# Kernel optimization log

Measured on AMD Instinct MI355X. Metric: run time of the kernel, lower is better.

Reference implementation:

```python
import jax, jax.numpy as jnp
import numpy as np

B, S, H, NH, NE = 4, 1024, 256, 4, 4
D = H // NH  # head_unit = 64
EPS = 1e-8


def layernorm(x, g, b):
    m = jnp.mean(x, axis=-1, keepdims=True)
    v = jnp.mean((x - m) ** 2, axis=-1, keepdims=True)
    return (x - m) / jnp.sqrt(v + EPS) * g + b


def setup_inputs() -> dict:
    key = jax.random.key(0)
    ks = jax.random.split(key, 18)
    sc = 0.05
    return {
        "x": jax.random.normal(ks[0], (B, S, H), jnp.float32),
        # MoEMultiHead params
        "hl_w": jax.random.normal(ks[1], (NH, D, H), jnp.float32) * sc,   # head_layer weights (out,in)
        "hl_b": jax.random.normal(ks[2], (NH, D), jnp.float32) * sc,
        "wq": jax.random.normal(ks[3], (NH, NE, D, D), jnp.float32) * sc,  # w_q[i*NH+j] -> wq[i,j]
        "wk": jax.random.normal(ks[4], (NH, D, D), jnp.float32) * sc,
        "wv": jax.random.normal(ks[5], (NH, D, D), jnp.float32) * sc,
        "gate_w": jax.random.normal(ks[6], (NH, NE, NE * D), jnp.float32) * sc,
        "gate_b": jax.random.normal(ks[7], (NH, NE), jnp.float32) * sc,
        "ln_g": jnp.ones((D,), jnp.float32),
        "ln_b": jnp.zeros((D,), jnp.float32),
        # FFN params (built inside forward in torch; materialized here)
        "fc1_w": jax.random.normal(ks[8], (D, D), jnp.float32) * sc,
        "fc1_b": jax.random.normal(ks[9], (D,), jnp.float32) * sc,
        "fc2_w": jax.random.normal(ks[10], (D, D), jnp.float32) * sc,
        "fc2_b": jax.random.normal(ks[11], (D,), jnp.float32) * sc,
        "fnorm_g": jnp.ones((D,), jnp.float32),
        "fnorm_b": jnp.zeros((D,), jnp.float32),
        "fgate_w": jax.random.normal(ks[12], (NH, H), jnp.float32) * sc,
    }


def reference(x, hl_w, hl_b, wq, wk, wv, gate_w, gate_b, ln_g, ln_b,
              fc1_w, fc1_b, fc2_w, fc2_b, fnorm_g, fnorm_b, fgate_w):
    b, s, h = x.shape
    nh, d, _ = wk.shape
    ne = wq.shape[1]
    # per-head projection of full hidden -> head_unit  (B, NH, S, D)
    sx = jnp.einsum('bsh,ndh->bnsd', x, hl_w) + hl_b[None, :, None, :]
    pad = sx == 0  # padding mask, same for all experts
    # per-(head, expert) q; per-head k, v
    q = jnp.einsum('bnsd,neod->bneso', sx, wq)       # (B,NH,NE,S,D)
    k = jnp.einsum('bnsd,nod->bnso', sx, wk)         # (B,NH,S,D)
    v = jnp.einsum('bnsd,nod->bnso', sx, wv)
    causal = jnp.where(jnp.tril(jnp.ones((s, s), bool)), 0.0, -jnp.inf).astype(x.dtype)
    # NOTE: original MULTIPLIES by sqrt(head_unit) (bug-faithful)
    scores = jnp.einsum('bnesd,bntd->bnest', q, k) * (d ** 0.5) + causal
    att = jax.nn.softmax(scores, axis=-1)
    qkv = jnp.einsum('bnest,bntd->bnesd', att, v)
    qkv = jnp.where(pad[:, :, None], 0.0, qkv)
    # concat experts along feature dim: (B,NH,S,NE*D)
    out = jnp.transpose(qkv, (0, 1, 3, 2, 4)).reshape(b, nh, s, ne * d)
    gs = jax.nn.softmax(jnp.einsum('bnsf,nef->bnse', out, gate_w) + gate_b[None, :, None, :], axis=-1)
    mixed = jnp.einsum('bnsed,bnse->bnsd', out.reshape(b, nh, s, ne, d), gs)
    # bug-faithful residual: split_x[i] indexes the BATCH dim with head index i
    resid = sx[jnp.arange(nh), jnp.arange(nh)]  # (NH, S, D), broadcast over batch
    hn = layernorm(mixed + resid, ln_g, ln_b)   # (B,NH,S,D); dropout inactive (p=0)
    f_n = jnp.transpose(hn, (0, 2, 1, 3)).reshape(b, s, h)
    # ---- FFN (fresh module in torch; deterministic params here) ----
    fx = f_n.reshape(b, s, nh, d)  # torch.split along feature dim
    pm = fx == 0
    hx = jnp.where(pm, 0.0, fx @ fc1_w.T + fc1_b)
    hx = jax.nn.relu(hx)
    hx = jnp.where(pm, 0.0, hx @ fc2_w.T + fc2_b)
    hx = layernorm(hx + fx, fnorm_g, fnorm_b)
    fout = hx.reshape(b, s, h)
    fg = jax.nn.softmax(fout @ fgate_w.T, axis=-1)  # (B,S,NH)
    return (fout.reshape(b, s, nh, d) * fg[..., None]).reshape(b, s, h)
```

## Files before the change

### kernel.cpp

```cpp
#include <hip/hip_runtime.h>
#include <math.h>

typedef unsigned short u16;
typedef __attribute__((ext_vector_type(8))) unsigned short us8;
typedef __attribute__((ext_vector_type(4))) unsigned short us4;
typedef __attribute__((ext_vector_type(8))) short bf16x8;
typedef __attribute__((ext_vector_type(4))) float f32x4;

constexpr int B_ = 4, S_ = 1024, H_ = 256, NH_ = 4, NE_ = 4, D_ = 64;
constexpr float EPS_ = 1e-8f;

__device__ __forceinline__ u16 f2bf(float f){
  unsigned u = __float_as_uint(f);
  unsigned rnd = 0x7fffu + ((u>>16)&1u);
  return (u16)((u + rnd)>>16);
}
__device__ __forceinline__ float bf2f(u16 u){ return __uint_as_float(((unsigned)u)<<16); }
__device__ __forceinline__ us4 pack4(float4 a){
  us4 r; r[0]=f2bf(a.x); r[1]=f2bf(a.y); r[2]=f2bf(a.z); r[3]=f2bf(a.w);
  return r;
}
#define MFMA16(a,b,c) __builtin_amdgcn_mfma_f32_16x16x32_bf16((bf16x8)(a),(bf16x8)(b),(c),0,0,0)

__global__ __launch_bounds__(256) void k_sx(const float* __restrict__ x, const float* __restrict__ hlw,
                                            const float* __restrict__ hlb,
                                            float* __restrict__ sx, u16* __restrict__ sxb){
  int mt = blockIdx.x >> 3, nt = blockIdx.x & 7;
  int tid = threadIdx.x, w = tid>>6, l = tid&63, lr = l>>4, lc = l&15;
  __shared__ u16 Xs[64*64];
  __shared__ u16 Ws[32*64];
  const int swl = (lc&7)<<3;
  f32x4 acc[2] = {{0,0,0,0},{0,0,0,0}};
  for(int ks=0; ks<4; ++ks){
    __syncthreads();
    #pragma unroll
    for(int it=0; it<4; ++it){
      int g = tid + it*256; int row = g>>4, c4 = (g&15)*4;
      float4 a = *(const float4*)(x + ((size_t)(mt*64+row))*H_ + ks*64 + c4);
      *(us4*)&Xs[row*64 + (c4 ^ ((row&7)<<3))] = pack4(a);
    }
    #pragma unroll
    for(int it=0; it<2; ++it){
      int g = tid + it*256; int row = g>>4, c4 = (g&15)*4;
      float4 a = *(const float4*)(hlw + ((size_t)(nt*32+row))*H_ + ks*64 + c4);
      *(us4*)&Ws[row*64 + (c4 ^ ((row&7)<<3))] = pack4(a);
    }
    __syncthreads();
    bf16x8 a0 = *(const bf16x8*)&Xs[(w*16+lc)*64 + ((lr*8   ) ^ swl)];
    bf16x8 a1 = *(const bf16x8*)&Xs[(w*16+lc)*64 + ((lr*8+32) ^ swl)];
    #pragma unroll
    for(int j=0;j<2;j++){
      const u16* wr = &Ws[(j*16+lc)*64];
      bf16x8 b0 = *(const bf16x8*)(wr + ((lr*8   ) ^ swl));
      bf16x8 b1 = *(const bf16x8*)(wr + ((lr*8+32) ^ swl));
      acc[j] = MFMA16(a0,b0,acc[j]);
      acc[j] = MFMA16(a1,b1,acc[j]);
    }
  }
  #pragma unroll
  for(int j=0;j<2;j++){
    int col = nt*32 + j*16 + lc;
    int n = col>>6, d = col&63;
    float bias = hlb[col];
    #pragma unroll
    for(int r=0;r<4;r++){
      int m = mt*64 + w*16 + lr*4 + r;
      int b = m>>10, s = m&1023;
      float v = acc[j][r] + bias;
      size_t idx = ((size_t)(b*NH_+n)*S_+s)*D_ + d;
      sx[idx] = v; sxb[idx] = f2bf(v);
    }
  }
}

__global__ __launch_bounds__(256) void k_qkv(const u16* __restrict__ sxb, const float* __restrict__ wq,
            const float* __restrict__ wk, const float* __restrict__ wv,
            u16* __restrict__ qb, u16* __restrict__ kbf, u16* __restrict__ vbT){
  int bid = blockIdx.x;
  int half = bid&1, mt = (bid>>1)&63, n = bid>>7;
  int tid = threadIdx.x, w = tid>>6, l = tid&63, lr = l>>4, lc = l&15;
  __shared__ u16 As[64*64];
  __shared__ u16 Ws[192*64];
  const int swl = (lc&7)<<3;
  int b = (mt*64)>>10, s0 = (mt*64)&1023;
  {
    int sr = tid>>3, sc = (tid&7)*8, sw = (sr&7)<<3;
    const u16* base = sxb + ((size_t)(b*NH_+n)*S_ + s0)*D_;
    *(us8*)&As[ sr     *64 + (sc ^ sw)] = *(const us8*)(base + (size_t) sr    *D_ + sc);
    *(us8*)&As[(sr+32)*64 + (sc ^ sw)] = *(const us8*)(base + (size_t)(sr+32)*D_ + sc);
  }
  #pragma unroll
  for(int it=0; it<12; ++it){
    int g = tid + it*256; int row = g>>4, c4 = (g&15)*4;
    int o = half*192 + row;
    const float* src;
    if(o < 256)      src = wq + ((size_t)((n*NE_ + (o>>6))*D_ + (o&63)))*D_;
    else if(o < 320) src = wk + ((size_t)(n*D_ + (o-256)))*D_;
    else             src = wv + ((size_t)(n*D_ + (o-320)))*D_;
    float4 a = *(const float4*)(src + c4);
    *(us4*)&Ws[row*64 + (c4 ^ ((row&7)<<3))] = pack4(a);
  }
  __syncthreads();
  bf16x8 a0 = *(const bf16x8*)&As[(w*16+lc)*64 + ((lr*8   ) ^ swl)];
  bf16x8 a1 = *(const bf16x8*)&As[(w*16+lc)*64 + ((lr*8+32) ^ swl)];
  f32x4 acc[12];
  #pragma unroll
  for(int j=0;j<12;j++) acc[j] = (f32x4){0,0,0,0};
  #pragma unroll
  for(int j=0;j<12;j++){
    const u16* wr = &Ws[(j*16+lc)*64];
    bf16x8 b0 = *(const bf16x8*)(wr + ((lr*8   ) ^ swl));
    bf16x8 b1 = *(const bf16x8*)(wr + ((lr*8+32) ^ swl));
    acc[j] = MFMA16(a0,b0,acc[j]);
    acc[j] = MFMA16(a1,b1,acc[j]);
  }
  #pragma unroll
  for(int j=0;j<12;j++){
    int o = half*192 + j*16 + lc;
    #pragma unroll
    for(int r=0;r<4;r++){
      int s = s0 + w*16 + lr*4 + r;
      float v = acc[j][r];
      if(o < 256){
        int e = o>>6, d = o&63;
        qb[((size_t)((b*NH_+n)*NE_+e)*S_ + s)*D_ + d] = f2bf(v*11.5415603f);
      } else if(o < 320){
        kbf[((size_t)(b*NH_+n)*S_ + s)*D_ + (o-256)] = f2bf(v);
      } else {
        int d = o-320;
        vbT[((size_t)(b*NH_+n)*D_ + d)*S_ + s] = f2bf(v);
      }
    }
  }
}

__global__ __launch_bounds__(256,4) void k_attn(const u16* __restrict__ qb, const u16* __restrict__ kb,
        const u16* __restrict__ vbT, const u16* __restrict__ sxb, u16* __restrict__ attoutb){
  int bid = blockIdx.x;
  int head = bid & 63, idx = bid >> 6;
  int g = idx>>2, pos = idx&3;
  int qt = (g&1) ? (15 - (g>>1) - 2*pos) : ((g>>1) + 2*pos);
  int bq = head>>2, e = head&3;
  int tid = threadIdx.x, w = tid>>6, l = tid&63, lr = l>>4, lc = l&15;
  __shared__ u16 Ks[2][64*64];
  __shared__ u16 VT[2][64*64];
  __shared__ u16 Pb[4][16*64];
  const u16* kh = kb  + (size_t)bq*S_*D_;
  const u16* vh = vbT + (size_t)bq*D_*S_;
  const int swl = (lc&7)<<3;
  const int sr = tid>>3, sc = (tid&7)*8, sw = (sr&7)<<3;

  const u16* qrow = qb + ((size_t)head*S_ + qt*64 + w*16 + lc)*D_;
  bf16x8 qf0 = *(const bf16x8*)(qrow + lr*8);
  bf16x8 qf1 = *(const bf16x8*)(qrow + lr*8 + 32);
  f32x4 Oa[4];
  #pragma unroll
  for(int j=0;j<4;j++) Oa[j] = (f32x4){0,0,0,0};
  float m_i = -INFINITY, l_i = 0.f;

  us8 rg[4];
  {
    rg[0] = *(const us8*)(kh + (size_t) sr    *D_ + sc);
    rg[1] = *(const us8*)(kh + (size_t)(sr+32)*D_ + sc);
    rg[2] = *(const us8*)(vh + (size_t) sr    *S_ + sc);
    rg[3] = *(const us8*)(vh + (size_t)(sr+32)*S_ + sc);
    *(us8*)&Ks[0][ sr    *64 + (sc ^ sw)] = rg[0];
    *(us8*)&Ks[0][(sr+32)*64 + (sc ^ sw)] = rg[1];
    *(us8*)&VT[0][ sr    *64 + (sc ^ sw)] = rg[2];
    *(us8*)&VT[0][(sr+32)*64 + (sc ^ sw)] = rg[3];
  }
  for(int kt=0; kt<=qt; ++kt){
    int cur = kt&1;
    __syncthreads();
    bool more = kt < qt;
    if(more){
      rg[0] = *(const us8*)(kh + ((size_t)(kt+1)*64 +  sr    )*D_ + sc);
      rg[1] = *(const us8*)(kh + ((size_t)(kt+1)*64 + (sr+32))*D_ + sc);
      rg[2] = *(const us8*)(vh + (size_t) sr    *S_ + (kt+1)*64 + sc);
      rg[3] = *(const us8*)(vh + (size_t)(sr+32)*S_ + (kt+1)*64 + sc);
    }
    f32x4 Sa[4];
    __builtin_amdgcn_s_setprio(1);
    #pragma unroll
    for(int j=0;j<4;j++){
      const u16* kr = &Ks[cur][(j*16+lc)*64];
      bf16x8 a0 = *(const bf16x8*)(kr + ((lr*8   ) ^ swl));
      bf16x8 a1 = *(const bf16x8*)(kr + ((lr*8+32) ^ swl));
      f32x4 z = (f32x4){0,0,0,0};
      z = MFMA16(a0,qf0,z);
      z = MFMA16(a1,qf1,z);
      Sa[j] = z;
    }
    __builtin_amdgcn_s_setprio(0);
    if(kt==qt){
      int q = w*16 + lc;
      #pragma unroll
      for(int j=0;j<4;j++)
        #pragma unroll
        for(int r=0;r<4;r++)
          if(j*16 + lr*4 + r > q) Sa[j][r] = -INFINITY;
    }
    float mx0 = fmaxf(fmaxf(Sa[0][0],Sa[0][1]),fmaxf(Sa[0][2],Sa[0][3]));
    float mx1 = fmaxf(fmaxf(Sa[1][0],Sa[1][1]),fmaxf(Sa[1][2],Sa[1][3]));
    float mx2 = fmaxf(fmaxf(Sa[2][0],Sa[2][1]),fmaxf(Sa[2][2],Sa[2][3]));
    float mx3 = fmaxf(fmaxf(Sa[3][0],Sa[3][1]),fmaxf(Sa[3][2],Sa[3][3]));
    float mx = fmaxf(fmaxf(mx0,mx1),fmaxf(mx2,mx3));
    mx = fmaxf(mx, __shfl_xor(mx,16));
    mx = fmaxf(mx, __shfl_xor(mx,32));
    float mn = fmaxf(m_i, mx);
    float scale = exp2f(m_i - mn);
    #pragma unroll
    for(int j=0;j<4;j++)
      #pragma unroll
      for(int r=0;r<4;r++) Sa[j][r] = exp2f(Sa[j][r] - mn);
    float rs0 = (Sa[0][0]+Sa[0][1]) + (Sa[0][2]+Sa[0][3]);
    float rs1 = (Sa[1][0]+Sa[1][1]) + (Sa[1][2]+Sa[1][3]);
    float rs2 = (Sa[2][0]+Sa[2][1]) + (Sa[2][2]+Sa[2][3]);
    float rs3 = (Sa[3][0]+Sa[3][1]) + (Sa[3][2]+Sa[3][3]);
    float rs = (rs0+rs1) + (rs2+rs3);
    rs += __shfl_xor(rs,16);
    rs += __shfl_xor(rs,32);
    l_i = l_i*scale + rs;
    m_i = mn;
    #pragma unroll
    for(int jd=0;jd<4;jd++)
      #pragma unroll
      for(int r=0;r<4;r++) Oa[jd][r] *= scale;
    #pragma unroll
    for(int j=0;j<4;j++){
      us4 pk;
      #pragma unroll
      for(int r=0;r<4;r++) pk[r] = f2bf(Sa[j][r]);
      *(us4*)&Pb[w][lc*64 + ((j*16+lr*4) ^ swl)] = pk;
    }
    asm volatile("s_waitcnt lgkmcnt(0)" ::: "memory");
    bf16x8 pB0 = *(const bf16x8*)&Pb[w][lc*64 + ((lr*8   ) ^ swl)];
    bf16x8 pB1 = *(const bf16x8*)&Pb[w][lc*64 + ((lr*8+32) ^ swl)];
    __builtin_amdgcn_s_setprio(1);
    #pragma unroll
    for(int jd=0;jd<4;jd++){
      const u16* vr = &VT[cur][(jd*16+lc)*64];
      bf16x8 v0 = *(const bf16x8*)(vr + ((lr*8   ) ^ swl));
      bf16x8 v1 = *(const bf16x8*)(vr + ((lr*8+32) ^ swl));
      Oa[jd] = MFMA16(v0,pB0,Oa[jd]);
      Oa[jd] = MFMA16(v1,pB1,Oa[jd]);
    }
    __builtin_amdgcn_s_setprio(0);
    if(more){
      int nb = cur^1;
      *(us8*)&Ks[nb][ sr    *64 + (sc ^ sw)] = rg[0];
      *(us8*)&Ks[nb][(sr+32)*64 + (sc ^ sw)] = rg[1];
      *(us8*)&VT[nb][ sr    *64 + (sc ^ sw)] = rg[2];
      *(us8*)&VT[nb][(sr+32)*64 + (sc ^ sw)] = rg[3];
    }
  }
  int qg = qt*64 + w*16 + lc;
  float inv = 1.f/l_i;
  const u16* sxp = sxb + ((size_t)bq*S_ + qg)*D_;
  u16* op = attoutb + ((size_t)bq*S_ + qg)*(NE_*D_) + e*D_;
  #pragma unroll
  for(int jd=0;jd<4;jd++){
    int d0 = jd*16 + lr*4;
    us4 sxv = *(const us4*)(sxp + d0);
    us4 ov;
    #pragma unroll
    for(int r=0;r<4;r++){
      float o = Oa[jd][r]*inv;
      ov[r] = ((sxv[r]&0x7fff)==0) ? (u16)0 : f2bf(o);
    }
    *(us4*)(op + d0) = ov;
  }
}

__global__ __launch_bounds__(256) void k_tail(const u16* __restrict__ attoutb, const float* __restrict__ gw,
      const float* __restrict__ gb, const float* __restrict__ sx,
      const float* __restrict__ lng, const float* __restrict__ lnb,
      const float* __restrict__ w1g, const float* __restrict__ b1g,
      const float* __restrict__ w2g, const float* __restrict__ b2g,
      const float* __restrict__ fng, const float* __restrict__ fnb,
      const float* __restrict__ fgw, float* __restrict__ out){
  int bid = blockIdx.x;
  int gs0 = bid*16, b = gs0>>10, s0 = gs0&1023;
  int tid = threadIdx.x;
  int row = tid>>4, l16 = tid&15;
  int w = tid>>6, l = tid&63, lr = l>>4, lc = l&15;
  __shared__ float Fx[64][64];
  __shared__ u16 FnB[64*64];
  __shared__ u16 W1[64*64], W2[64*64], H1[64*64];
  __shared__ float Red[4][16][4];

  #pragma unroll
  for(int g2=0; g2<2; ++g2){
    int g = tid*2+g2; int r2 = g>>3, c0 = (g&7)*8;
    float4 a = *(const float4*)(w1g + r2*64 + c0), bb = *(const float4*)(w1g + r2*64 + c0 + 4);
    us8 p; 
    p[0]=f2bf(a.x);p[1]=f2bf(a.y);p[2]=f2bf(a.z);p[3]=f2bf(a.w);
    p[4]=f2bf(bb.x);p[5]=f2bf(bb.y);p[6]=f2bf(bb.z);p[7]=f2bf(bb.w);
    *(us8*)&W1[r2*64 + (c0 ^ ((r2&7)<<3))] = p;
    a = *(const float4*)(w2g + r2*64 + c0); bb = *(const float4*)(w2g + r2*64 + c0 + 4);
    p[0]=f2bf(a.x);p[1]=f2bf(a.y);p[2]=f2bf(a.z);p[3]=f2bf(a.w);
    p[4]=f2bf(bb.x);p[5]=f2bf(bb.y);p[6]=f2bf(bb.z);p[7]=f2bf(bb.w);
    *(us8*)&W2[r2*64 + (c0 ^ ((r2&7)<<3))] = p;
  }
  const int d0 = l16*4;
  for(int n=0;n<NH_;++n){
    f32x4 o[4];
    const u16* ar = attoutb + ((size_t)(b*NH_+n)*S_ + s0 + row)*(NE_*D_);
    #pragma unroll
    for(int e=0;e<4;e++){
      us4 t = *(const us4*)(ar + e*64 + d0);
      #pragma unroll
      for(int k=0;k<4;k++) o[e][k] = bf2f(t[k]);
    }
    float lg4[4];
    #pragma unroll
    for(int eg=0; eg<4; ++eg){
      const float* gr = gw + (size_t)(n*NE_+eg)*(NE_*D_);
      float p = 0.f;
      #pragma unroll
      for(int e=0;e<4;e++){
        f32x4 g4 = *(const f32x4*)(gr + e*64 + d0);
        p += o[e][0]*g4[0] + o[e][1]*g4[1] + o[e][2]*g4[2] + o[e][3]*g4[3];
      }
      #pragma unroll
      for(int off=1; off<16; off<<=1) p += __shfl_xor(p, off);
      lg4[eg] = p + gb[n*NE_+eg];
    }
    float mx = fmaxf(fmaxf(lg4[0],lg4[1]),fmaxf(lg4[2],lg4[3]));
    float se = 0.f;
    #pragma unroll
    for(int eg=0;eg<4;eg++){ lg4[eg]=__expf(lg4[eg]-mx); se+=lg4[eg]; }
    float inv = 1.f/se;
    f32x4 res = *(const f32x4*)(sx + ((size_t)(n*NH_+n)*S_ + s0 + row)*D_ + d0);
    float tv[4];
    #pragma unroll
    for(int k=0;k<4;k++){
      float mixk = o[0][k]*lg4[0] + o[1][k]*lg4[1] + o[2][k]*lg4[2] + o[3][k]*lg4[3];
      tv[k] = mixk*inv + res[k];
    }
    float sum = tv[0]+tv[1]+tv[2]+tv[3];
    #pragma unroll
    for(int off=1; off<16; off<<=1) sum += __shfl_xor(sum, off);
    float mean = sum*(1.f/64.f);
    float vs = 0.f;
    #pragma unroll
    for(int k=0;k<4;k++){ float d = tv[k]-mean; vs += d*d; }
    #pragma unroll
    for(int off=1; off<16; off<<=1) vs += __shfl_xor(vs, off);
    float rstd = rsqrtf(vs*(1.f/64.f)+EPS_);
    f32x4 lgv = *(const f32x4*)(lng + d0);
    f32x4 lbv = *(const f32x4*)(lnb + d0);
    int hr = n*16+row;
    us4 pk;
    f32x4 yv;
    #pragma unroll
    for(int k=0;k<4;k++){
      float y = (tv[k]-mean)*rstd*lgv[k] + lbv[k];
      yv[k] = y; pk[k] = f2bf(y);
    }
    *(f32x4*)&Fx[hr][d0] = yv;
    *(us4*)&FnB[hr*64 + (d0 ^ ((hr&7)<<3))] = pk;
  }
  __syncthreads();
  const int swl = (lc&7)<<3;
  bf16x8 a0 = *(const bf16x8*)&FnB[(w*16+lc)*64 + ((lr*8   ) ^ swl)];
  bf16x8 a1 = *(const bf16x8*)&FnB[(w*16+lc)*64 + ((lr*8+32) ^ swl)];
  f32x4 acc1[4];
  #pragma unroll
  for(int jn=0;jn<4;jn++) acc1[jn] = (f32x4){0,0,0,0};
  #pragma unroll
  for(int jn=0;jn<4;jn++){
    const u16* wr = &W1[(jn*16+lc)*64];
    bf16x8 b0 = *(const bf16x8*)(wr + ((lr*8   ) ^ swl));
    bf16x8 b1 = *(const bf16x8*)(wr + ((lr*8+32) ^ swl));
    acc1[jn] = MFMA16(a0,b0,acc1[jn]);
    acc1[jn] = MFMA16(a1,b1,acc1[jn]);
  }
  #pragma unroll
  for(int jn=0;jn<4;jn++){
    int dout = jn*16+lc;
    float bias = b1g[dout];
    #pragma unroll
    for(int rr=0;rr<4;rr++){
      int hr = w*16 + lr*4 + rr;
      float v = acc1[jn][rr] + bias;
      v = (Fx[hr][dout]==0.f) ? 0.f : v;
      v = fmaxf(v, 0.f);
      H1[hr*64 + (dout ^ ((hr&7)<<3))] = f2bf(v);
    }
  }
  __syncthreads();
  a0 = *(const bf16x8*)&H1[(w*16+lc)*64 + ((lr*8   ) ^ swl)];
  a1 = *(const bf16x8*)&H1[(w*16+lc)*64 + ((lr*8+32) ^ swl)];
  f32x4 acc2[4];
  #pragma unroll
  for(int jn=0;jn<4;jn++) acc2[jn] = (f32x4){0,0,0,0};
  #pragma unroll
  for(int jn=0;jn<4;jn++){
    const u16* wr = &W2[(jn*16+lc)*64];
    bf16x8 b0 = *(const bf16x8*)(wr + ((lr*8   ) ^ swl));
    bf16x8 b1 = *(const bf16x8*)(wr + ((lr*8+32) ^ swl));
    acc2[jn] = MFMA16(a0,b0,acc2[jn]);
    acc2[jn] = MFMA16(a1,b1,acc2[jn]);
  }
  float tv2[4][4];
  #pragma unroll
  for(int jn=0;jn<4;jn++){
    int dout = jn*16+lc;
    float bias = b2g[dout];
    #pragma unroll
    for(int rr=0;rr<4;rr++){
      int hr = w*16 + lr*4 + rr;
      float fx = Fx[hr][dout];
      float v = acc2[jn][rr] + bias;
      v = (fx==0.f) ? 0.f : v;
      tv2[jn][rr] = v + fx;
    }
  }
  float sum_r[4], vs_r[4];
  #pragma unroll
  for(int rr=0;rr<4;rr++) sum_r[rr] = tv2[0][rr]+tv2[1][rr]+tv2[2][rr]+tv2[3][rr];
  #pragma unroll
  for(int off=1; off<16; off<<=1)
    #pragma unroll
    for(int rr=0;rr<4;rr++) sum_r[rr] += __shfl_xor(sum_r[rr], off);
  float mean_r[4];
  #pragma unroll
  for(int rr=0;rr<4;rr++) mean_r[rr] = sum_r[rr]*(1.f/64.f);
  #pragma unroll
  for(int rr=0;rr<4;rr++){
    float a = tv2[0][rr]-mean_r[rr], b2v = tv2[1][rr]-mean_r[rr];
    float c = tv2[2][rr]-mean_r[rr], d = tv2[3][rr]-mean_r[rr];
    vs_r[rr] = a*a + b2v*b2v + c*c + d*d;
  }
  #pragma unroll
  for(int off=1; off<16; off<<=1)
    #pragma unroll
    for(int rr=0;rr<4;rr++) vs_r[rr] += __shfl_xor(vs_r[rr], off);
  float y2[4][4];
  #pragma unroll
  for(int jn=0;jn<4;jn++){
    int dout = jn*16+lc;
    float g = fng[dout], bb = fnb[dout];
    #pragma unroll
    for(int rr=0;rr<4;rr++){
      float rstd = rsqrtf(vs_r[rr]*(1.f/64.f)+EPS_);
      y2[jn][rr] = (tv2[jn][rr]-mean_r[rr])*rstd*g + bb;
    }
  }
  float fg4[4][4];
  #pragma unroll
  for(int j=0;j<4;j++)
    #pragma unroll
    for(int jn=0;jn<4;jn++)
      fg4[j][jn] = fgw[(size_t)j*H_ + w*64 + jn*16 + lc];
  float pj[4][4];
  #pragma unroll
  for(int j=0;j<4;j++)
    #pragma unroll
    for(int rr=0;rr<4;rr++)
      pj[j][rr] = y2[0][rr]*fg4[j][0] + y2[1][rr]*fg4[j][1] + y2[2][rr]*fg4[j][2] + y2[3][rr]*fg4[j][3];
  #pragma unroll
  for(int off=1; off<16; off<<=1)
    #pragma unroll
    for(int j=0;j<4;j++)
      #pragma unroll
      for(int rr=0;rr<4;rr++) pj[j][rr] += __shfl_xor(pj[j][rr], off);
  if(lc==0){
    #pragma unroll
    for(int rr=0;rr<4;rr++)
      #pragma unroll
      for(int j=0;j<4;j++) Red[w][lr*4+rr][j] = pj[j][rr];
  }
  __syncthreads();
  #pragma unroll
  for(int rr=0;rr<4;rr++){
    int srow = lr*4+rr;
    float lgf[4];
    #pragma unroll
    for(int j=0;j<4;j++) lgf[j] = Red[0][srow][j]+Red[1][srow][j]+Red[2][srow][j]+Red[3][srow][j];
    float mx2 = fmaxf(fmaxf(lgf[0],lgf[1]),fmaxf(lgf[2],lgf[3]));
    float se2 = 0.f;
    #pragma unroll
    for(int j=0;j<4;j++){ lgf[j]=__expf(lgf[j]-mx2); se2+=lgf[j]; }
    float gsn = lgf[w]/se2;
    float* op = out + ((size_t)(gs0 + srow))*H_ + w*64;
    #pragma unroll
    for(int jn=0;jn<4;jn++) op[jn*16+lc] = y2[jn][rr]*gsn;
  }
}

extern "C" void kernel_launch(void* const* d_in, const int* in_sizes, int n_in,
                              void* d_out, int out_size, void* d_ws, size_t ws_size,
                              hipStream_t stream){
  const float* x      = (const float*)d_in[0];
  const float* hl_w   = (const float*)d_in[1];
  const float* hl_b   = (const float*)d_in[2];
  const float* wq     = (const float*)d_in[3];
  const float* wk     = (const float*)d_in[4];
  const float* wv     = (const float*)d_in[5];
  const float* gate_w = (const float*)d_in[6];
  const float* gate_b = (const float*)d_in[7];
  const float* ln_g   = (const float*)d_in[8];
  const float* ln_b   = (const float*)d_in[9];
  const float* fc1_w  = (const float*)d_in[10];
  const float* fc1_b  = (const float*)d_in[11];
  const float* fc2_w  = (const float*)d_in[12];
  const float* fc2_b  = (const float*)d_in[13];
  const float* fnorm_g= (const float*)d_in[14];
  const float* fnorm_b= (const float*)d_in[15];
  const float* fgate_w= (const float*)d_in[16];

  const size_t NSD = (size_t)B_*NH_*S_*D_;
  float* ws      = (float*)d_ws;
  float* sx      = ws;
  u16*   sxb     = (u16*)(sx + NSD);
  u16*   attoutb = sxb + NSD;
  u16*   qb      = attoutb + NSD*NE_;
  u16*   kbf     = qb + NSD*NE_;
  u16*   vbT     = kbf + NSD;

  k_sx  <<<512,  256, 0, stream>>>(x, hl_w, hl_b, sx, sxb);
  k_qkv <<<512,  256, 0, stream>>>(sxb, wq, wk, wv, qb, kbf, vbT);
  k_attn<<<1024, 256, 0, stream>>>(qb, kbf, vbT, sxb, attoutb);
  k_tail<<<256,  256, 0, stream>>>(attoutb, gate_w, gate_b, sx, ln_g, ln_b,
                                   fc1_w, fc1_b, fc2_w, fc2_b,
                                   fnorm_g, fnorm_b, fgate_w, (float*)d_out);
}
```

Baseline: 65.50 us.

## Share K/V tiles across two experts per attention block with 32 query rows per wave

Each attention block now serves two experts of the same batch-head. Each wave handles 32 query rows of one expert instead of 16, so every K/V tile staged in shared memory is reused by twice as many MFMAs. The grid is halved to 512 blocks and the qt-to-block mapping is rebuilt for causal load balance. The costs are higher register pressure (launch bounds lowered to 2 blocks per SIMD), a doubled P buffer in LDS, and fewer blocks to hide latency.

Result: slower. 73.96 us (+12.9%).

```diff
diff --git a/kernel.cpp b/kernel.cpp
--- a/kernel.cpp
+++ b/kernel.cpp
@@ -83,8 +83,7 @@
   __shared__ u16 Ws[192*64];
   const int swl = (lc&7)<<3;
   int b = (mt*64)>>10, s0 = (mt*64)&1023;
-  {
-    int sr = tid>>3, sc = (tid&7)*8, sw = (sr&7)<<3;
+  { int sr = tid>>3, sc = (tid&7)*8, sw = (sr&7)<<3;
     const u16* base = sxb + ((size_t)(b*NH_+n)*S_ + s0)*D_;
     *(us8*)&As[ sr     *64 + (sc ^ sw)] = *(const us8*)(base + (size_t) sr    *D_ + sc);
     *(us8*)&As[(sr+32)*64 + (sc ^ sw)] = *(const us8*)(base + (size_t)(sr+32)*D_ + sc);
@@ -134,29 +133,35 @@
   }
 }
 
-__global__ __launch_bounds__(256,4) void k_attn(const u16* __restrict__ qb, const u16* __restrict__ kb,
+__global__ __launch_bounds__(256,2) void k_attn(const u16* __restrict__ qb, const u16* __restrict__ kb,
         const u16* __restrict__ vbT, const u16* __restrict__ sxb, u16* __restrict__ attoutb){
   int bid = blockIdx.x;
-  int head = bid & 63, idx = bid >> 6;
-  int g = idx>>2, pos = idx&3;
-  int qt = (g&1) ? (15 - (g>>1) - 2*pos) : ((g>>1) + 2*pos);
-  int bq = head>>2, e = head&3;
+  int idx = bid>>5, rem = bid&31, bq = rem>>1, eh = rem&1;
+  int qt = (idx<8) ? ((idx&3)*2 + (idx>>2))
+                   : 15 - ((idx&3)*2 + ((idx>>2)&1));
   int tid = threadIdx.x, w = tid>>6, l = tid&63, lr = l>>4, lc = l&15;
+  int e = 2*eh + (w>>1), h = w&1;
   __shared__ u16 Ks[2][64*64];
   __shared__ u16 VT[2][64*64];
-  __shared__ u16 Pb[4][16*64];
+  __shared__ u16 Pb[4][32*64];
   const u16* kh = kb  + (size_t)bq*S_*D_;
   const u16* vh = vbT + (size_t)bq*D_*S_;
   const int swl = (lc&7)<<3;
   const int sr = tid>>3, sc = (tid&7)*8, sw = (sr&7)<<3;
 
-  const u16* qrow = qb + ((size_t)head*S_ + qt*64 + w*16 + lc)*D_;
-  bf16x8 qf0 = *(const bf16x8*)(qrow + lr*8);
-  bf16x8 qf1 = *(const bf16x8*)(qrow + lr*8 + 32);
-  f32x4 Oa[4];
-  #pragma unroll
-  for(int j=0;j<4;j++) Oa[j] = (f32x4){0,0,0,0};
-  float m_i = -INFINITY, l_i = 0.f;
+  bf16x8 qf[2][2];
+  #pragma unroll
+  for(int jql=0;jql<2;jql++){
+    const u16* qrow = qb + ((size_t)(bq*NE_+e)*S_ + qt*64 + (2*h+jql)*16 + lc)*D_;
+    qf[jql][0] = *(const bf16x8*)(qrow + lr*8);
+    qf[jql][1] = *(const bf16x8*)(qrow + lr*8 + 32);
+  }
+  f32x4 Oa[2][4];
+  #pragma unroll
+  for(int jql=0;jql<2;jql++)
+    #pragma unroll
+    for(int j=0;j<4;j++) Oa[jql][j] = (f32x4){0,0,0,0};
+  float m_i[2] = {-INFINITY,-INFINITY}, l_i[2] = {0.f,0.f};
 
   us8 rg[4];
   {
@@ -179,71 +184,87 @@
       rg[2] = *(const us8*)(vh + (size_t) sr    *S_ + (kt+1)*64 + sc);
       rg[3] = *(const us8*)(vh + (size_t)(sr+32)*S_ + (kt+1)*64 + sc);
     }
-    f32x4 Sa[4];
+    f32x4 Sa[2][4];
     __builtin_amdgcn_s_setprio(1);
     #pragma unroll
     for(int j=0;j<4;j++){
       const u16* kr = &Ks[cur][(j*16+lc)*64];
       bf16x8 a0 = *(const bf16x8*)(kr + ((lr*8   ) ^ swl));
       bf16x8 a1 = *(const bf16x8*)(kr + ((lr*8+32) ^ swl));
-      f32x4 z = (f32x4){0,0,0,0};
-      z = MFMA16(a0,qf0,z);
-      z = MFMA16(a1,qf1,z);
-      Sa[j] = z;
+      #pragma unroll
+      for(int jql=0;jql<2;jql++){
+        f32x4 z = (f32x4){0,0,0,0};
+        z = MFMA16(a0,qf[jql][0],z);
+        z = MFMA16(a1,qf[jql][1],z);
+        Sa[jql][j] = z;
+      }
     }
     __builtin_amdgcn_s_setprio(0);
     if(kt==qt){
-      int q = w*16 + lc;
+      #pragma unroll
+      for(int jql=0;jql<2;jql++){
+        int q = (2*h+jql)*16 + lc;
+        #pragma unroll
+        for(int j=0;j<4;j++)
+          #pragma unroll
+          for(int r=0;r<4;r++)
+            if(j*16 + lr*4 + r > q) Sa[jql][j][r] = -INFINITY;
+      }
+    }
+    #pragma unroll
+    for(int jql=0;jql<2;jql++){
+      float mx0 = fmaxf(fmaxf(Sa[jql][0][0],Sa[jql][0][1]),fmaxf(Sa[jql][0][2],Sa[jql][0][3]));
+      float mx1 = fmaxf(fmaxf(Sa[jql][1][0],Sa[jql][1][1]),fmaxf(Sa[jql][1][2],Sa[jql][1][3]));
+      float mx2 = fmaxf(fmaxf(Sa[jql][2][0],Sa[jql][2][1]),fmaxf(Sa[jql][2][2],Sa[jql][2][3]));
+      float mx3 = fmaxf(fmaxf(Sa[jql][3][0],Sa[jql][3][1]),fmaxf(Sa[jql][3][2],Sa[jql][3][3]));
+      float mx = fmaxf(fmaxf(mx0,mx1),fmaxf(mx2,mx3));
+      mx = fmaxf(mx, __shfl_xor(mx,16));
+      mx = fmaxf(mx, __shfl_xor(mx,32));
+      float mn = fmaxf(m_i[jql], mx);
+      float scale = exp2f(m_i[jql] - mn);
       #pragma unroll
       for(int j=0;j<4;j++)
         #pragma unroll
-        for(int r=0;r<4;r++)
-          if(j*16 + lr*4 + r > q) Sa[j][r] = -INFINITY;
-    }
-    float mx0 = fmaxf(fmaxf(Sa[0][0],Sa[0][1]),fmaxf(Sa[0][2],Sa[0][3]));
-    float mx1 = fmaxf(fmaxf(Sa[1][0],Sa[1][1]),fmaxf(Sa[1][2],Sa[1][3]));
-    float mx2 = fmaxf(fmaxf(Sa[2][0],Sa[2][1]),fmaxf(Sa[2][2],Sa[2][3]));
-    float mx3 = fmaxf(fmaxf(Sa[3][0],Sa[3][1]),fmaxf(Sa[3][2],Sa[3][3]));
-    float mx = fmaxf(fmaxf(mx0,mx1),fmaxf(mx2,mx3));
-    mx = fmaxf(mx, __shfl_xor(mx,16));
-    mx = fmaxf(mx, __shfl_xor(mx,32));
-    float mn = fmaxf(m_i, mx);
-    float scale = exp2f(m_i - mn);
-    #pragma unroll
-    for(int j=0;j<4;j++)
-      #pragma unroll
-      for(int r=0;r<4;r++) Sa[j][r] = exp2f(Sa[j][r] - mn);
-    float rs0 = (Sa[0][0]+Sa[0][1]) + (Sa[0][2]+Sa[0][3]);
-    float rs1 = (Sa[1][0]+Sa[1][1]) + (Sa[1][2]+Sa[1][3]);
-    float rs2 = (Sa[2][0]+Sa[2][1]) + (Sa[2][2]+Sa[2][3]);
-    float rs3 = (Sa[3][0]+Sa[3][1]) + (Sa[3][2]+Sa[3][3]);
-    float rs = (rs0+rs1) + (rs2+rs3);
-    rs += __shfl_xor(rs,16);
-    rs += __shfl_xor(rs,32);
-    l_i = l_i*scale + rs;
-    m_i = mn;
-    #pragma unroll
-    for(int jd=0;jd<4;jd++)
-      #pragma unroll
-      for(int r=0;r<4;r++) Oa[jd][r] *= scale;
-    #pragma unroll
-    for(int j=0;j<4;j++){
-      us4 pk;
-      #pragma unroll
-      for(int r=0;r<4;r++) pk[r] = f2bf(Sa[j][r]);
-      *(us4*)&Pb[w][lc*64 + ((j*16+lr*4) ^ swl)] = pk;
+        for(int r=0;r<4;r++) Sa[jql][j][r] = exp2f(Sa[jql][j][r] - mn);
+      float rs0 = (Sa[jql][0][0]+Sa[jql][0][1]) + (Sa[jql][0][2]+Sa[jql][0][3]);
+      float rs1 = (Sa[jql][1][0]+Sa[jql][1][1]) + (Sa[jql][1][2]+Sa[jql][1][3]);
+      float rs2 = (Sa[jql][2][0]+Sa[jql][2][1]) + (Sa[jql][2][2]+Sa[jql][2][3]);
+      float rs3 = (Sa[jql][3][0]+Sa[jql][3][1]) + (Sa[jql][3][2]+Sa[jql][3][3]);
+      float rs = (rs0+rs1) + (rs2+rs3);
+      rs += __shfl_xor(rs,16);
+      rs += __shfl_xor(rs,32);
+      l_i[jql] = l_i[jql]*scale + rs;
+      m_i[jql] = mn;
+      #pragma unroll
+      for(int jd=0;jd<4;jd++)
+        #pragma unroll
+        for(int r=0;r<4;r++) Oa[jql][jd][r] *= scale;
+      #pragma unroll
+      for(int j=0;j<4;j++){
+        us4 pk;
+        #pragma unroll
+        for(int r=0;r<4;r++) pk[r] = f2bf(Sa[jql][j][r]);
+        *(us4*)&Pb[w][(jql*16+lc)*64 + ((j*16+lr*4) ^ swl)] = pk;
+      }
     }
     asm volatile("s_waitcnt lgkmcnt(0)" ::: "memory");
-    bf16x8 pB0 = *(const bf16x8*)&Pb[w][lc*64 + ((lr*8   ) ^ swl)];
-    bf16x8 pB1 = *(const bf16x8*)&Pb[w][lc*64 + ((lr*8+32) ^ swl)];
+    bf16x8 pB[2][2];
+    #pragma unroll
+    for(int jql=0;jql<2;jql++){
+      pB[jql][0] = *(const bf16x8*)&Pb[w][(jql*16+lc)*64 + ((lr*8   ) ^ swl)];
+      pB[jql][1] = *(const bf16x8*)&Pb[w][(jql*16+lc)*64 + ((lr*8+32) ^ swl)];
+    }
     __builtin_amdgcn_s_setprio(1);
     #pragma unroll
     for(int jd=0;jd<4;jd++){
       const u16* vr = &VT[cur][(jd*16+lc)*64];
       bf16x8 v0 = *(const bf16x8*)(vr + ((lr*8   ) ^ swl));
       bf16x8 v1 = *(const bf16x8*)(vr + ((lr*8+32) ^ swl));
-      Oa[jd] = MFMA16(v0,pB0,Oa[jd]);
-      Oa[jd] = MFMA16(v1,pB1,Oa[jd]);
+      #pragma unroll
+      for(int jql=0;jql<2;jql++){
+        Oa[jql][jd] = MFMA16(v0,pB[jql][0],Oa[jql][jd]);
+        Oa[jql][jd] = MFMA16(v1,pB[jql][1],Oa[jql][jd]);
+      }
     }
     __builtin_amdgcn_s_setprio(0);
     if(more){
@@ -254,21 +275,24 @@
       *(us8*)&VT[nb][(sr+32)*64 + (sc ^ sw)] = rg[3];
     }
   }
-  int qg = qt*64 + w*16 + lc;
-  float inv = 1.f/l_i;
-  const u16* sxp = sxb + ((size_t)bq*S_ + qg)*D_;
-  u16* op = attoutb + ((size_t)bq*S_ + qg)*(NE_*D_) + e*D_;
-  #pragma unroll
-  for(int jd=0;jd<4;jd++){
-    int d0 = jd*16 + lr*4;
-    us4 sxv = *(const us4*)(sxp + d0);
-    us4 ov;
-    #pragma unroll
-    for(int r=0;r<4;r++){
-      float o = Oa[jd][r]*inv;
-      ov[r] = ((sxv[r]&0x7fff)==0) ? (u16)0 : f2bf(o);
-    }
-    *(us4*)(op + d0) = ov;
+  #pragma unroll
+  for(int jql=0;jql<2;jql++){
+    int qg = qt*64 + (2*h+jql)*16 + lc;
+    float inv = 1.f/l_i[jql];
+    const u16* sxp = sxb + ((size_t)bq*S_ + qg)*D_;
+    u16* op = attoutb + ((size_t)bq*S_ + qg)*(NE_*D_) + e*D_;
+    #pragma unroll
+    for(int jd=0;jd<4;jd++){
+      int d0 = jd*16 + lr*4;
+      us4 sxv = *(const us4*)(sxp + d0);
+      us4 ov;
+      #pragma unroll
+      for(int r=0;r<4;r++){
+        float o = Oa[jql][jd][r]*inv;
+        ov[r] = ((sxv[r]&0x7fff)==0) ? (u16)0 : f2bf(o);
+      }
+      *(us4*)(op + d0) = ov;
+    }
   }
 }
 
@@ -293,7 +317,7 @@
   for(int g2=0; g2<2; ++g2){
     int g = tid*2+g2; int r2 = g>>3, c0 = (g&7)*8;
     float4 a = *(const float4*)(w1g + r2*64 + c0), bb = *(const float4*)(w1g + r2*64 + c0 + 4);
-    us8 p; 
+    us8 p;
     p[0]=f2bf(a.x);p[1]=f2bf(a.y);p[2]=f2bf(a.z);p[3]=f2bf(a.w);
     p[4]=f2bf(bb.x);p[5]=f2bf(bb.y);p[6]=f2bf(bb.z);p[7]=f2bf(bb.w);
     *(us8*)&W1[r2*64 + (c0 ^ ((r2&7)<<3))] = p;
@@ -522,7 +546,7 @@
 
   k_sx  <<<512,  256, 0, stream>>>(x, hl_w, hl_b, sx, sxb);
   k_qkv <<<512,  256, 0, stream>>>(sxb, wq, wk, wv, qb, kbf, vbT);
-  k_attn<<<1024, 256, 0, stream>>>(qb, kbf, vbT, sxb, attoutb);
+  k_attn<<<512,  256, 0, stream>>>(qb, kbf, vbT, sxb, attoutb);
   k_tail<<<256,  256, 0, stream>>>(attoutb, gate_w, gate_b, sx, ln_g, ln_b,
                                    fc1_w, fc1_b, fc2_w, fc2_b,
                                    fnorm_g, fnorm_b, fgate_w, (float*)d_out);
```
